# Optimization experiments

Hardware: AMD Instinct MI355X
Metric: run time of the kernel (lower is better)

The kernel has to match this reference:

```python
import jax, jax.numpy as jnp
import numpy as np

BOX = 256
SIGMA = 1.5
KS = 9  # int(ceil(6*sigma)), made odd
N_POINTS = 20000
N_NEURONS = 32
N_LAYERS = 3
LATENT = 8
BATCH = 16


def _make_kernel2(ks, sigma):
    ax = np.arange(ks) - ks // 2
    yy, xx = np.meshgrid(ax, ax, indexing='ij')
    k = np.exp(-(xx ** 2 + yy ** 2) / (2.0 * sigma ** 2))
    return (k / k.sum()).astype(np.float32)


def setup_inputs() -> dict:
    key = jax.random.key(0)
    ks = jax.random.split(key, 16)
    def n(k, shape, scale=1.0):
        return scale * jax.random.normal(k, shape, dtype=jnp.float32)
    return {
        'z': n(ks[0], (BATCH, LATENT)),
        'r': n(ks[1], (BATCH, 3, 3)),
        'pos': 0.1 * (jax.random.uniform(ks[2], (N_POINTS, 3), dtype=jnp.float32) - 0.5),
        'amp': 0.1 * jnp.ones((1,), jnp.float32),
        'linamp1_W': n(ks[3], (N_NEURONS, 4), 0.3),
        'ampblock_W': n(ks[4], (N_LAYERS, N_NEURONS, N_NEURONS), 0.1),
        'ampblock_b': n(ks[5], (N_LAYERS, N_NEURONS), 0.05),
        'linamp2_W': n(ks[6], (1, N_NEURONS), 0.1),
        'linamp2_b': n(ks[7], (1,), 0.05),
        'lin0_W': n(ks[8], (N_NEURONS, 3 + LATENT - 1), 0.3),
        'deform_W': n(ks[9], (N_LAYERS, N_NEURONS, N_NEURONS), 0.1),
        'deform_b': n(ks[10], (N_LAYERS, N_NEURONS), 0.05),
        'lin1a_W': n(ks[11], (3, N_NEURONS), 0.2),
        'lin1b_W': n(ks[12], (3, 3), 0.2),
        'k2': jnp.asarray(_make_kernel2(KS, SIGMA)),
        'd': 1,
    }


def _res_mlp(x, Ws, bs):
    # residual blocks: x <- relu(x @ W^T + b) + x
    for i in range(Ws.shape[0]):
        x = jax.nn.relu(x @ Ws[i].T + bs[i]) + x
    return x


def _splat(proj, amps, k2):
    # Gaussian-kernel splat of points onto [B, BOX, BOX] images.
    # proj: [B,P,2] coords in ~[-0.5, 0.5]; amps: [B,P]; k2: [KS,KS]
    B, P, _ = proj.shape
    ks = k2.shape[0]
    half = ks // 2
    pix = (proj + 0.5) * (BOX - 1)
    cx = jnp.round(pix[..., 0]).astype(jnp.int32)
    cy = jnp.round(pix[..., 1]).astype(jnp.int32)
    offs = jnp.arange(ks, dtype=jnp.int32) - half
    oy, ox = jnp.meshgrid(offs, offs, indexing='ij')
    xx = cx[:, :, None] + ox.reshape(-1)[None, None, :]   # [B,P,ks*ks]
    yy = cy[:, :, None] + oy.reshape(-1)[None, None, :]
    w = amps[:, :, None] * k2.reshape(-1)[None, None, :]
    valid = (xx >= 0) & (xx < BOX) & (yy >= 0) & (yy < BOX)
    bidx = jnp.arange(B, dtype=jnp.int32)[:, None, None]
    flat = jnp.where(valid, (bidx * BOX + yy) * BOX + xx, 0)
    img = jnp.zeros((B * BOX * BOX,), proj.dtype).at[flat.reshape(-1)].add(
        jnp.where(valid, w, jnp.zeros_like(w)).reshape(-1))
    return img.reshape(B, BOX, BOX)


def _forward(z, r, pos, amp, linamp1_W, ampblock_W, ampblock_b, linamp2_W,
             linamp2_b, lin0_W, deform_W, deform_b, lin1a_W, lin1b_W, k2, d):
    B = z.shape[0]
    P = pos.shape[0]
    posi = jnp.broadcast_to(pos[None], (B, P, 3))
    # amplitude head (diff_conf=True): last latent channel per point
    conf_a = jnp.broadcast_to(z[:, -1:][:, None, :], (B, P, 1))
    a = jnp.concatenate([posi, conf_a], axis=-1) @ linamp1_W.T
    a = _res_mlp(a, ampblock_W, ampblock_b)
    amp_corr = jax.nn.sigmoid(a @ linamp2_W.T + linamp2_b)  # [B,P,1]
    # deformation head on remaining latent channels
    if d > 0:
        conf = jnp.broadcast_to(z[:, :-1][:, None, :], (B, P, z.shape[1] - 1))
        res = jnp.concatenate([posi, conf], axis=-1) @ lin0_W.T
        res = _res_mlp(res, deform_W, deform_b)
        res = jnp.tanh(res @ lin1a_W.T)
        res = res @ lin1b_W.T
        pos_def = posi + res
    else:
        res = jnp.zeros_like(posi)
        pos_def = posi
    # project rotated points to 2D
    proj_pos = jnp.einsum('bij,bpj->bpi', r, pos_def)[..., :2]
    amps = amp * amp_corr[..., 0]  # [B,P]
    proj_im = _splat(proj_pos, amps, k2)
    return proj_im, pos_def, res, amp_corr


def reference(z, r, pos, amp, linamp1_W, ampblock_W, ampblock_b, linamp2_W,
              linamp2_b, lin0_W, deform_W, deform_b, lin1a_W, lin1b_W, k2, d):
    return _forward(z, r, pos, amp, linamp1_W, ampblock_W, ampblock_b,
                    linamp2_W, linamp2_b, lin0_W, deform_W, deform_b,
                    lin1a_W, lin1b_W, k2, d)
```

## Files before the change

### kernel.cpp

```cpp
#include <hip/hip_runtime.h>

#define BOX   256
#define KS    9
#define HALF  4
#define NPTS  20000
#define NB    16
#define NLAT  8
#define CANW  264
#define NPBLK 1250
#define CANVAS_ELEMS (NB * CANW * CANW)

typedef _Float16 half8   __attribute__((ext_vector_type(8)));
typedef float    floatx4 __attribute__((ext_vector_type(4)));

__global__ __launch_bounds__(256) void point_kernel(
    const float* __restrict__ z, const float* __restrict__ r,
    const float* __restrict__ pos, const float* __restrict__ amp,
    const float* __restrict__ linamp1_W, const float* __restrict__ ampblock_W,
    const float* __restrict__ ampblock_b, const float* __restrict__ linamp2_W,
    const float* __restrict__ linamp2_b, const float* __restrict__ lin0_W,
    const float* __restrict__ deform_W, const float* __restrict__ deform_b,
    const float* __restrict__ lin1a_W, const float* __restrict__ lin1b_W,
    const int* __restrict__ dflag,
    float* __restrict__ canvas, float* __restrict__ pos_def_out,
    float* __restrict__ res_out, float* __restrict__ amp_corr_out)
{
    const int lane = threadIdx.x & 63;
    const int n    = lane & 15;
    const int quad = lane >> 4;
    const int s    = blockIdx.x * 4 + (threadIdx.x >> 6);
    const int d    = *dflag;
    const float ampv = amp[0];
    const float l2b  = linamp2_b[0];
    const floatx4 zero = {0.f, 0.f, 0.f, 0.f};

    int   bb[4];
    float px[4], py[4], pz[4];
    half8 bfa[4], bfd[4];
    #pragma unroll
    for (int g = 0; g < 4; ++g) {
        const int base_bp = s * 64 + g * 16;
        const int b = base_bp / NPTS;
        const int p = base_bp - b * NPTS + n;
        bb[g] = b;
        px[g] = pos[3 * p + 0];
        py[g] = pos[3 * p + 1];
        pz[g] = pos[3 * p + 2];
        float zl[NLAT];
        #pragma unroll
        for (int k = 0; k < NLAT; ++k) zl[k] = z[b * NLAT + k];
        half8 t;
        #pragma unroll
        for (int j = 0; j < 8; ++j) t[j] = (_Float16)0.f;
        bfa[g] = t; bfd[g] = t;
        if (quad == 0) {
            bfa[g][0] = (_Float16)px[g]; bfa[g][1] = (_Float16)py[g];
            bfa[g][2] = (_Float16)pz[g]; bfa[g][3] = (_Float16)zl[7];
            bfd[g][0] = (_Float16)px[g]; bfd[g][1] = (_Float16)py[g];
            bfd[g][2] = (_Float16)pz[g]; bfd[g][3] = (_Float16)zl[0];
            bfd[g][4] = (_Float16)zl[1]; bfd[g][5] = (_Float16)zl[2];
            bfd[g][6] = (_Float16)zl[3]; bfd[g][7] = (_Float16)zl[4];
        } else if (quad == 1) {
            bfd[g][0] = (_Float16)zl[5]; bfd[g][1] = (_Float16)zl[6];
        }
    }

    float xB[4][8];
    {
        floatx4 w0 = *(const floatx4*)(linamp1_W + n * 4);
        floatx4 w1 = *(const floatx4*)(linamp1_W + (n + 16) * 4);
        half8 a0, a1;
        #pragma unroll
        for (int j = 0; j < 8; ++j) { a0[j] = (_Float16)0.f; a1[j] = (_Float16)0.f; }
        if (quad == 0) {
            #pragma unroll
            for (int j = 0; j < 4; ++j) {
                a0[j] = (_Float16)w0[j];
                a1[j] = (_Float16)w1[j];
            }
        }
        #pragma unroll
        for (int g = 0; g < 4; ++g) {
            floatx4 c0 = __builtin_amdgcn_mfma_f32_16x16x32_f16(a0, bfa[g], zero, 0, 0, 0);
            floatx4 c1 = __builtin_amdgcn_mfma_f32_16x16x32_f16(a1, bfa[g], zero, 0, 0, 0);
            #pragma unroll
            for (int rr = 0; rr < 4; ++rr) { xB[g][rr] = c0[rr]; xB[g][4 + rr] = c1[rr]; }
        }
    }
    #pragma unroll
    for (int l = 0; l < 3; ++l) {
        const float* W = ampblock_W + l * 1024;
        floatx4 f00 = *(const floatx4*)(W + n * 32 + quad * 4);
        floatx4 f01 = *(const floatx4*)(W + n * 32 + 16 + quad * 4);
        floatx4 f10 = *(const floatx4*)(W + (n + 16) * 32 + quad * 4);
        floatx4 f11 = *(const floatx4*)(W + (n + 16) * 32 + 16 + quad * 4);
        half8 a0, a1;
        #pragma unroll
        for (int j = 0; j < 4; ++j) {
            a0[j] = (_Float16)f00[j]; a0[4 + j] = (_Float16)f01[j];
            a1[j] = (_Float16)f10[j]; a1[4 + j] = (_Float16)f11[j];
        }
        floatx4 b0 = *(const floatx4*)(ampblock_b + l * 32 + quad * 4);
        floatx4 b1 = *(const floatx4*)(ampblock_b + l * 32 + 16 + quad * 4);
        #pragma unroll
        for (int g = 0; g < 4; ++g) {
            half8 hf;
            #pragma unroll
            for (int j = 0; j < 8; ++j) hf[j] = (_Float16)xB[g][j];
            floatx4 d0 = __builtin_amdgcn_mfma_f32_16x16x32_f16(a0, hf, zero, 0, 0, 0);
            floatx4 d1 = __builtin_amdgcn_mfma_f32_16x16x32_f16(a1, hf, zero, 0, 0, 0);
            #pragma unroll
            for (int rr = 0; rr < 4; ++rr) {
                xB[g][rr]     += fmaxf(d0[rr] + b0[rr], 0.f);
                xB[g][4 + rr] += fmaxf(d1[rr] + b1[rr], 0.f);
            }
        }
    }
    float corr[4];
    {
        floatx4 wa = *(const floatx4*)(linamp2_W + quad * 4);
        floatx4 wb = *(const floatx4*)(linamp2_W + 16 + quad * 4);
        #pragma unroll
        for (int g = 0; g < 4; ++g) {
            float sd = 0.f;
            #pragma unroll
            for (int rr = 0; rr < 4; ++rr) sd += wa[rr] * xB[g][rr] + wb[rr] * xB[g][4 + rr];
            sd += __shfl_xor(sd, 16);
            sd += __shfl_xor(sd, 32);
            corr[g] = 1.f / (1.f + __expf(-(sd + l2b)));
        }
    }

    float r0[4] = {0.f,0.f,0.f,0.f}, r1[4] = {0.f,0.f,0.f,0.f}, r2[4] = {0.f,0.f,0.f,0.f};
    if (d > 0) {
        {
            float c0v[8], c1v[8];
            #pragma unroll
            for (int j = 0; j < 8; ++j) { c0v[j] = 0.f; c1v[j] = 0.f; }
            const float* row0 = lin0_W + n * 10;
            const float* row1 = lin0_W + (n + 16) * 10;
            if (quad == 0) {
                #pragma unroll
                for (int j = 0; j < 8; ++j) { c0v[j] = row0[j]; c1v[j] = row1[j]; }
            } else if (quad == 1) {
                c0v[0] = row0[8]; c0v[1] = row0[9];
                c1v[0] = row1[8]; c1v[1] = row1[9];
            }
            half8 a0, a1;
            #pragma unroll
            for (int j = 0; j < 8; ++j) {
                a0[j] = (_Float16)c0v[j];
                a1[j] = (_Float16)c1v[j];
            }
            #pragma unroll
            for (int g = 0; g < 4; ++g) {
                floatx4 c0 = __builtin_amdgcn_mfma_f32_16x16x32_f16(a0, bfd[g], zero, 0, 0, 0);
                floatx4 c1 = __builtin_amdgcn_mfma_f32_16x16x32_f16(a1, bfd[g], zero, 0, 0, 0);
                #pragma unroll
                for (int rr = 0; rr < 4; ++rr) { xB[g][rr] = c0[rr]; xB[g][4 + rr] = c1[rr]; }
            }
        }
        #pragma unroll
        for (int l = 0; l < 3; ++l) {
            const float* W = deform_W + l * 1024;
            floatx4 f00 = *(const floatx4*)(W + n * 32 + quad * 4);
            floatx4 f01 = *(const floatx4*)(W + n * 32 + 16 + quad * 4);
            floatx4 f10 = *(const floatx4*)(W + (n + 16) * 32 + quad * 4);
            floatx4 f11 = *(const floatx4*)(W + (n + 16) * 32 + 16 + quad * 4);
            half8 a0, a1;
            #pragma unroll
            for (int j = 0; j < 4; ++j) {
                a0[j] = (_Float16)f00[j]; a0[4 + j] = (_Float16)f01[j];
                a1[j] = (_Float16)f10[j]; a1[4 + j] = (_Float16)f11[j];
            }
            floatx4 b0 = *(const floatx4*)(deform_b + l * 32 + quad * 4);
            floatx4 b1 = *(const floatx4*)(deform_b + l * 32 + 16 + quad * 4);
            #pragma unroll
            for (int g = 0; g < 4; ++g) {
                half8 hf;
                #pragma unroll
                for (int j = 0; j < 8; ++j) hf[j] = (_Float16)xB[g][j];
                floatx4 d0 = __builtin_amdgcn_mfma_f32_16x16x32_f16(a0, hf, zero, 0, 0, 0);
                floatx4 d1 = __builtin_amdgcn_mfma_f32_16x16x32_f16(a1, hf, zero, 0, 0, 0);
                #pragma unroll
                for (int rr = 0; rr < 4; ++rr) {
                    xB[g][rr]     += fmaxf(d0[rr] + b0[rr], 0.f);
                    xB[g][4 + rr] += fmaxf(d1[rr] + b1[rr], 0.f);
                }
            }
        }
        #pragma unroll
        for (int i = 0; i < 3; ++i) {
            floatx4 wa = *(const floatx4*)(lin1a_W + i * 32 + quad * 4);
            floatx4 wb = *(const floatx4*)(lin1a_W + i * 32 + 16 + quad * 4);
            const float lb0 = lin1b_W[0 * 3 + i];
            const float lb1 = lin1b_W[1 * 3 + i];
            const float lb2 = lin1b_W[2 * 3 + i];
            #pragma unroll
            for (int g = 0; g < 4; ++g) {
                float sd = 0.f;
                #pragma unroll
                for (int rr = 0; rr < 4; ++rr) sd += wa[rr] * xB[g][rr] + wb[rr] * xB[g][4 + rr];
                sd += __shfl_xor(sd, 16);
                sd += __shfl_xor(sd, 32);
                const float t3 = 1.f - 2.f / (__expf(2.f * sd) + 1.f);
                r0[g] = fmaf(t3, lb0, r0[g]);
                r1[g] = fmaf(t3, lb1, r1[g]);
                r2[g] = fmaf(t3, lb2, r2[g]);
            }
        }
    }

    #pragma unroll
    for (int g = 0; g < 4; ++g) {
        const int bp = s * 64 + g * 16 + n;
        const float pdx = px[g] + r0[g], pdy = py[g] + r1[g], pdz = pz[g] + r2[g];
        if (quad == 0) {
            pos_def_out[3 * bp + 0] = pdx;
            pos_def_out[3 * bp + 1] = pdy;
            pos_def_out[3 * bp + 2] = pdz;
        } else if (quad == 1) {
            res_out[3 * bp + 0] = r0[g];
            res_out[3 * bp + 1] = r1[g];
            res_out[3 * bp + 2] = r2[g];
        } else if (quad == 2) {
            amp_corr_out[bp] = corr[g];
        } else {
            const float* rb = r + bb[g] * 9;
            const float pjx = rb[0] * pdx + rb[1] * pdy + rb[2] * pdz;
            const float pjy = rb[3] * pdx + rb[4] * pdy + rb[5] * pdz;
            const int cx = (int)rintf((pjx + 0.5f) * (float)(BOX - 1));
            const int cy = (int)rintf((pjy + 0.5f) * (float)(BOX - 1));
            if (cx >= -HALF && cx <= BOX - 1 + HALF &&
                cy >= -HALF && cy <= BOX - 1 + HALF) {
                atomicAdd(canvas + ((size_t)bb[g] * CANW + (cy + HALF)) * CANW + (cx + HALF),
                          ampv * corr[g]);
            }
        }
    }
}

__global__ __launch_bounds__(256) void conv_kernel(
    const float* __restrict__ canvas, const float* __restrict__ k2,
    float* __restrict__ img)
{
    __shared__ float t_lds[24][256];
    const int x  = threadIdx.x;
    const int b  = blockIdx.x >> 4;
    const int y0 = (blockIdx.x & 15) * 16;

    float g[KS];
    #pragma unroll
    for (int i = 0; i < KS; ++i) {
        float sg = 0.f;
        #pragma unroll
        for (int j = 0; j < KS; ++j) sg += k2[i * KS + j];
        g[i] = sg;
    }

    const float* cb = canvas + (size_t)b * CANW * CANW;
    #pragma unroll 4
    for (int rr = 0; rr < 24; ++rr) {
        const float* row = cb + (size_t)(y0 + rr) * CANW;
        float s = 0.f;
        #pragma unroll
        for (int i = 0; i < KS; ++i) s = fmaf(g[i], row[x + (KS - 1) - i], s);
        t_lds[rr][x] = s;
    }
    __syncthreads();

    float* ib = img + ((size_t)b * BOX + y0) * BOX;
    #pragma unroll 4
    for (int yy = 0; yy < 16; ++yy) {
        float s = 0.f;
        #pragma unroll
        for (int i = 0; i < KS; ++i) s = fmaf(g[i], t_lds[yy + (KS - 1) - i][x], s);
        ib[yy * BOX + x] = s;
    }
}

extern "C" void kernel_launch(void* const* d_in, const int* in_sizes, int n_in,
                              void* d_out, int out_size, void* d_ws, size_t ws_size,
                              hipStream_t stream) {
    const float* z          = (const float*)d_in[0];
    const float* r          = (const float*)d_in[1];
    const float* pos        = (const float*)d_in[2];
    const float* amp        = (const float*)d_in[3];
    const float* linamp1_W  = (const float*)d_in[4];
    const float* ampblock_W = (const float*)d_in[5];
    const float* ampblock_b = (const float*)d_in[6];
    const float* linamp2_W  = (const float*)d_in[7];
    const float* linamp2_b  = (const float*)d_in[8];
    const float* lin0_W     = (const float*)d_in[9];
    const float* deform_W   = (const float*)d_in[10];
    const float* deform_b   = (const float*)d_in[11];
    const float* lin1a_W    = (const float*)d_in[12];
    const float* lin1b_W    = (const float*)d_in[13];
    const float* k2         = (const float*)d_in[14];
    const int*   dflag      = (const int*)d_in[15];

    float* out = (float*)d_out;
    float* img          = out;
    float* pos_def_out  = out + (size_t)NB * BOX * BOX;
    float* res_out      = pos_def_out + (size_t)NB * NPTS * 3;
    float* amp_corr_out = res_out + (size_t)NB * NPTS * 3;

    float* canvas = (float*)d_ws;

    hipMemsetAsync(canvas, 0, (size_t)CANVAS_ELEMS * sizeof(float), stream);

    point_kernel<<<NPBLK, 256, 0, stream>>>(
        z, r, pos, amp, linamp1_W, ampblock_W, ampblock_b, linamp2_W,
        linamp2_b, lin0_W, deform_W, deform_b, lin1a_W, lin1b_W, dflag,
        canvas, pos_def_out, res_out, amp_corr_out);

    conv_kernel<<<NB * 16, 256, 0, stream>>>(canvas, k2, img);
}
```

Baseline: 151.6 us.

## Pre-pack MLP weights to fp16 in a prep kernel and halve points per wave

Adds a small prep kernel that converts and permutes all MLP weight matrices into fp16 MFMA-ready layout in workspace, so the point kernel loads half8 fragments directly instead of converting fp32 weights per wave. It also folds the bias into the MFMA accumulator input, uses packed cvt_pkrtz for the activation conversion, and processes 32 points per wave instead of 64, doubling the grid. The aim is less per-wave conversion work, lower register pressure and more parallelism. The cost is an extra kernel launch and more blocks that each reload the weights.

```diff
diff --git a/kernel.cpp b/kernel.cpp
--- a/kernel.cpp
+++ b/kernel.cpp
@@ -7,48 +7,80 @@
 #define NB    16
 #define NLAT  8
 #define CANW  264
-#define NPBLK 1250
+#define NPBLK 2500
 #define CANVAS_ELEMS (NB * CANW * CANW)
 
 typedef _Float16 half8   __attribute__((ext_vector_type(8)));
+typedef __fp16   fp16x2  __attribute__((ext_vector_type(2)));
 typedef float    floatx4 __attribute__((ext_vector_type(4)));
+
+#define WH_BYTES 16384
+
+__device__ __forceinline__ int perm_inv(int k) {
+    return ((k >> 2) & 1) * 16 + (k >> 3) * 4 + (k & 3);
+}
+
+__device__ __forceinline__ half8 pack8(const float x[8]) {
+    union { fp16x2 v2[4]; half8 v8; } u;
+    u.v2[0] = __builtin_amdgcn_cvt_pkrtz(x[0], x[1]);
+    u.v2[1] = __builtin_amdgcn_cvt_pkrtz(x[2], x[3]);
+    u.v2[2] = __builtin_amdgcn_cvt_pkrtz(x[4], x[5]);
+    u.v2[3] = __builtin_amdgcn_cvt_pkrtz(x[6], x[7]);
+    return u.v8;
+}
+
+__global__ __launch_bounds__(256) void prep_kernel(
+    const float* __restrict__ linamp1_W, const float* __restrict__ ampblock_W,
+    const float* __restrict__ lin0_W, const float* __restrict__ deform_W,
+    _Float16* __restrict__ wh)
+{
+    const int idx = blockIdx.x * 256 + threadIdx.x;
+    if (idx >= 8192) return;
+    const int mat = idx >> 10, rem = idx & 1023;
+    const int m = rem >> 5, k = rem & 31;
+    float v = 0.0f;
+    if (mat == 0)      { if (k < 4)  v = linamp1_W[m * 4 + k]; }
+    else if (mat <= 3) { v = ampblock_W[(mat - 1) * 1024 + m * 32 + perm_inv(k)]; }
+    else if (mat == 4) { if (k < 10) v = lin0_W[m * 10 + k]; }
+    else               { v = deform_W[(mat - 5) * 1024 + m * 32 + perm_inv(k)]; }
+    wh[idx] = (_Float16)v;
+}
 
 __global__ __launch_bounds__(256) void point_kernel(
     const float* __restrict__ z, const float* __restrict__ r,
     const float* __restrict__ pos, const float* __restrict__ amp,
-    const float* __restrict__ linamp1_W, const float* __restrict__ ampblock_W,
     const float* __restrict__ ampblock_b, const float* __restrict__ linamp2_W,
-    const float* __restrict__ linamp2_b, const float* __restrict__ lin0_W,
-    const float* __restrict__ deform_W, const float* __restrict__ deform_b,
+    const float* __restrict__ linamp2_b, const float* __restrict__ deform_b,
     const float* __restrict__ lin1a_W, const float* __restrict__ lin1b_W,
-    const int* __restrict__ dflag,
+    const int* __restrict__ dflag, const _Float16* __restrict__ wh,
     float* __restrict__ canvas, float* __restrict__ pos_def_out,
     float* __restrict__ res_out, float* __restrict__ amp_corr_out)
 {
     const int lane = threadIdx.x & 63;
     const int n    = lane & 15;
     const int quad = lane >> 4;
+    const int aoff = quad * 8;
     const int s    = blockIdx.x * 4 + (threadIdx.x >> 6);
     const int d    = *dflag;
     const float ampv = amp[0];
     const float l2b  = linamp2_b[0];
     const floatx4 zero = {0.f, 0.f, 0.f, 0.f};
 
-    int   bb[4];
-    float px[4], py[4], pz[4];
-    half8 bfa[4], bfd[4];
-    #pragma unroll
-    for (int g = 0; g < 4; ++g) {
-        const int base_bp = s * 64 + g * 16;
-        const int b = base_bp / NPTS;
-        const int p = base_bp - b * NPTS + n;
-        bb[g] = b;
+    const int base0 = s * 32;
+    const int b     = base0 / NPTS;
+
+    float zl[NLAT];
+    #pragma unroll
+    for (int k = 0; k < NLAT; ++k) zl[k] = z[b * NLAT + k];
+
+    float px[2], py[2], pz[2];
+    half8 bfa[2], bfd[2];
+    #pragma unroll
+    for (int g = 0; g < 2; ++g) {
+        const int p = base0 - b * NPTS + g * 16 + n;
         px[g] = pos[3 * p + 0];
         py[g] = pos[3 * p + 1];
         pz[g] = pos[3 * p + 2];
-        float zl[NLAT];
-        #pragma unroll
-        for (int k = 0; k < NLAT; ++k) zl[k] = z[b * NLAT + k];
         half8 t;
         #pragma unroll
         for (int j = 0; j < 8; ++j) t[j] = (_Float16)0.f;
@@ -65,22 +97,12 @@
         }
     }
 
-    float xB[4][8];
+    float xB[2][8];
     {
-        floatx4 w0 = *(const floatx4*)(linamp1_W + n * 4);
-        floatx4 w1 = *(const floatx4*)(linamp1_W + (n + 16) * 4);
-        half8 a0, a1;
-        #pragma unroll
-        for (int j = 0; j < 8; ++j) { a0[j] = (_Float16)0.f; a1[j] = (_Float16)0.f; }
-        if (quad == 0) {
-            #pragma unroll
-            for (int j = 0; j < 4; ++j) {
-                a0[j] = (_Float16)w0[j];
-                a1[j] = (_Float16)w1[j];
-            }
-        }
-        #pragma unroll
-        for (int g = 0; g < 4; ++g) {
+        half8 a0 = *(const half8*)(wh + n * 32 + aoff);
+        half8 a1 = *(const half8*)(wh + (n + 16) * 32 + aoff);
+        #pragma unroll
+        for (int g = 0; g < 2; ++g) {
             floatx4 c0 = __builtin_amdgcn_mfma_f32_16x16x32_f16(a0, bfa[g], zero, 0, 0, 0);
             floatx4 c1 = __builtin_amdgcn_mfma_f32_16x16x32_f16(a1, bfa[g], zero, 0, 0, 0);
             #pragma unroll
@@ -89,39 +111,29 @@
     }
     #pragma unroll
     for (int l = 0; l < 3; ++l) {
-        const float* W = ampblock_W + l * 1024;
-        floatx4 f00 = *(const floatx4*)(W + n * 32 + quad * 4);
-        floatx4 f01 = *(const floatx4*)(W + n * 32 + 16 + quad * 4);
-        floatx4 f10 = *(const floatx4*)(W + (n + 16) * 32 + quad * 4);
-        floatx4 f11 = *(const floatx4*)(W + (n + 16) * 32 + 16 + quad * 4);
-        half8 a0, a1;
-        #pragma unroll
-        for (int j = 0; j < 4; ++j) {
-            a0[j] = (_Float16)f00[j]; a0[4 + j] = (_Float16)f01[j];
-            a1[j] = (_Float16)f10[j]; a1[4 + j] = (_Float16)f11[j];
-        }
+        const _Float16* M = wh + (1 + l) * 1024;
+        half8 a0 = *(const half8*)(M + n * 32 + aoff);
+        half8 a1 = *(const half8*)(M + (n + 16) * 32 + aoff);
         floatx4 b0 = *(const floatx4*)(ampblock_b + l * 32 + quad * 4);
         floatx4 b1 = *(const floatx4*)(ampblock_b + l * 32 + 16 + quad * 4);
         #pragma unroll
-        for (int g = 0; g < 4; ++g) {
-            half8 hf;
-            #pragma unroll
-            for (int j = 0; j < 8; ++j) hf[j] = (_Float16)xB[g][j];
-            floatx4 d0 = __builtin_amdgcn_mfma_f32_16x16x32_f16(a0, hf, zero, 0, 0, 0);
-            floatx4 d1 = __builtin_amdgcn_mfma_f32_16x16x32_f16(a1, hf, zero, 0, 0, 0);
+        for (int g = 0; g < 2; ++g) {
+            half8 hf = pack8(xB[g]);
+            floatx4 d0 = __builtin_amdgcn_mfma_f32_16x16x32_f16(a0, hf, b0, 0, 0, 0);
+            floatx4 d1 = __builtin_amdgcn_mfma_f32_16x16x32_f16(a1, hf, b1, 0, 0, 0);
             #pragma unroll
             for (int rr = 0; rr < 4; ++rr) {
-                xB[g][rr]     += fmaxf(d0[rr] + b0[rr], 0.f);
-                xB[g][4 + rr] += fmaxf(d1[rr] + b1[rr], 0.f);
-            }
-        }
-    }
-    float corr[4];
+                xB[g][rr]     += fmaxf(d0[rr], 0.f);
+                xB[g][4 + rr] += fmaxf(d1[rr], 0.f);
+            }
+        }
+    }
+    float corr[2];
     {
         floatx4 wa = *(const floatx4*)(linamp2_W + quad * 4);
         floatx4 wb = *(const floatx4*)(linamp2_W + 16 + quad * 4);
         #pragma unroll
-        for (int g = 0; g < 4; ++g) {
+        for (int g = 0; g < 2; ++g) {
             float sd = 0.f;
             #pragma unroll
             for (int rr = 0; rr < 4; ++rr) sd += wa[rr] * xB[g][rr] + wb[rr] * xB[g][4 + rr];
@@ -131,29 +143,14 @@
         }
     }
 
-    float r0[4] = {0.f,0.f,0.f,0.f}, r1[4] = {0.f,0.f,0.f,0.f}, r2[4] = {0.f,0.f,0.f,0.f};
+    float r0[2] = {0.f, 0.f}, r1[2] = {0.f, 0.f}, r2[2] = {0.f, 0.f};
     if (d > 0) {
         {
-            float c0v[8], c1v[8];
-            #pragma unroll
-            for (int j = 0; j < 8; ++j) { c0v[j] = 0.f; c1v[j] = 0.f; }
-            const float* row0 = lin0_W + n * 10;
-            const float* row1 = lin0_W + (n + 16) * 10;
-            if (quad == 0) {
-                #pragma unroll
-                for (int j = 0; j < 8; ++j) { c0v[j] = row0[j]; c1v[j] = row1[j]; }
-            } else if (quad == 1) {
-                c0v[0] = row0[8]; c0v[1] = row0[9];
-                c1v[0] = row1[8]; c1v[1] = row1[9];
-            }
-            half8 a0, a1;
-            #pragma unroll
-            for (int j = 0; j < 8; ++j) {
-                a0[j] = (_Float16)c0v[j];
-                a1[j] = (_Float16)c1v[j];
-            }
-            #pragma unroll
-            for (int g = 0; g < 4; ++g) {
+            const _Float16* M = wh + 4 * 1024;
+            half8 a0 = *(const half8*)(M + n * 32 + aoff);
+            half8 a1 = *(const half8*)(M + (n + 16) * 32 + aoff);
+            #pragma unroll
+            for (int g = 0; g < 2; ++g) {
                 floatx4 c0 = __builtin_amdgcn_mfma_f32_16x16x32_f16(a0, bfd[g], zero, 0, 0, 0);
                 floatx4 c1 = __builtin_amdgcn_mfma_f32_16x16x32_f16(a1, bfd[g], zero, 0, 0, 0);
                 #pragma unroll
@@ -162,30 +159,20 @@
         }
         #pragma unroll
         for (int l = 0; l < 3; ++l) {
-            const float* W = deform_W + l * 1024;
-            floatx4 f00 = *(const floatx4*)(W + n * 32 + quad * 4);
-            floatx4 f01 = *(const floatx4*)(W + n * 32 + 16 + quad * 4);
-            floatx4 f10 = *(const floatx4*)(W + (n + 16) * 32 + quad * 4);
-            floatx4 f11 = *(const floatx4*)(W + (n + 16) * 32 + 16 + quad * 4);
-            half8 a0, a1;
-            #pragma unroll
-            for (int j = 0; j < 4; ++j) {
-                a0[j] = (_Float16)f00[j]; a0[4 + j] = (_Float16)f01[j];
-                a1[j] = (_Float16)f10[j]; a1[4 + j] = (_Float16)f11[j];
-            }
+            const _Float16* M = wh + (5 + l) * 1024;
+            half8 a0 = *(const half8*)(M + n * 32 + aoff);
+            half8 a1 = *(const half8*)(M + (n + 16) * 32 + aoff);
             floatx4 b0 = *(const floatx4*)(deform_b + l * 32 + quad * 4);
             floatx4 b1 = *(const floatx4*)(deform_b + l * 32 + 16 + quad * 4);
             #pragma unroll
-            for (int g = 0; g < 4; ++g) {
-                half8 hf;
-                #pragma unroll
-                for (int j = 0; j < 8; ++j) hf[j] = (_Float16)xB[g][j];
-                floatx4 d0 = __builtin_amdgcn_mfma_f32_16x16x32_f16(a0, hf, zero, 0, 0, 0);
-                floatx4 d1 = __builtin_amdgcn_mfma_f32_16x16x32_f16(a1, hf, zero, 0, 0, 0);
+            for (int g = 0; g < 2; ++g) {
+                half8 hf = pack8(xB[g]);
+                floatx4 d0 = __builtin_amdgcn_mfma_f32_16x16x32_f16(a0, hf, b0, 0, 0, 0);
+                floatx4 d1 = __builtin_amdgcn_mfma_f32_16x16x32_f16(a1, hf, b1, 0, 0, 0);
                 #pragma unroll
                 for (int rr = 0; rr < 4; ++rr) {
-                    xB[g][rr]     += fmaxf(d0[rr] + b0[rr], 0.f);
-                    xB[g][4 + rr] += fmaxf(d1[rr] + b1[rr], 0.f);
+                    xB[g][rr]     += fmaxf(d0[rr], 0.f);
+                    xB[g][4 + rr] += fmaxf(d1[rr], 0.f);
                 }
             }
         }
@@ -197,7 +184,7 @@
             const float lb1 = lin1b_W[1 * 3 + i];
             const float lb2 = lin1b_W[2 * 3 + i];
             #pragma unroll
-            for (int g = 0; g < 4; ++g) {
+            for (int g = 0; g < 2; ++g) {
                 float sd = 0.f;
                 #pragma unroll
                 for (int rr = 0; rr < 4; ++rr) sd += wa[rr] * xB[g][rr] + wb[rr] * xB[g][4 + rr];
@@ -212,8 +199,8 @@
     }
 
     #pragma unroll
-    for (int g = 0; g < 4; ++g) {
-        const int bp = s * 64 + g * 16 + n;
+    for (int g = 0; g < 2; ++g) {
+        const int bp = base0 + g * 16 + n;
         const float pdx = px[g] + r0[g], pdy = py[g] + r1[g], pdz = pz[g] + r2[g];
         if (quad == 0) {
             pos_def_out[3 * bp + 0] = pdx;
@@ -226,14 +213,14 @@
         } else if (quad == 2) {
             amp_corr_out[bp] = corr[g];
         } else {
-            const float* rb = r + bb[g] * 9;
+            const float* rb = r + b * 9;
             const float pjx = rb[0] * pdx + rb[1] * pdy + rb[2] * pdz;
             const float pjy = rb[3] * pdx + rb[4] * pdy + rb[5] * pdz;
             const int cx = (int)rintf((pjx + 0.5f) * (float)(BOX - 1));
             const int cy = (int)rintf((pjy + 0.5f) * (float)(BOX - 1));
             if (cx >= -HALF && cx <= BOX - 1 + HALF &&
                 cy >= -HALF && cy <= BOX - 1 + HALF) {
-                atomicAdd(canvas + ((size_t)bb[g] * CANW + (cy + HALF)) * CANW + (cx + HALF),
+                atomicAdd(canvas + ((size_t)b * CANW + (cy + HALF)) * CANW + (cx + HALF),
                           ampv * corr[g]);
             }
         }
@@ -305,14 +292,18 @@
     float* res_out      = pos_def_out + (size_t)NB * NPTS * 3;
     float* amp_corr_out = res_out + (size_t)NB * NPTS * 3;
 
-    float* canvas = (float*)d_ws;
-
-    hipMemsetAsync(canvas, 0, (size_t)CANVAS_ELEMS * sizeof(float), stream);
+    _Float16* wh     = (_Float16*)d_ws;
+    float*    canvas = (float*)((char*)d_ws + WH_BYTES);
+
+    (void)hipMemsetAsync(canvas, 0, (size_t)CANVAS_ELEMS * sizeof(float), stream);
+
+    prep_kernel<<<32, 256, 0, stream>>>(
+        linamp1_W, ampblock_W, lin0_W, deform_W, wh);
 
     point_kernel<<<NPBLK, 256, 0, stream>>>(
-        z, r, pos, amp, linamp1_W, ampblock_W, ampblock_b, linamp2_W,
-        linamp2_b, lin0_W, deform_W, deform_b, lin1a_W, lin1b_W, dflag,
-        canvas, pos_def_out, res_out, amp_corr_out);
+        z, r, pos, amp, ampblock_b, linamp2_W, linamp2_b, deform_b,
+        lin1a_W, lin1b_W, dflag, wh, canvas,
+        pos_def_out, res_out, amp_corr_out);
 
     conv_kernel<<<NB * 16, 256, 0, stream>>>(canvas, k2, img);
 }
```

Result: faster. 136.5 us (-9.9%).
